# Kernel optimization log

Hardware: AMD Instinct MI355X
Metric: run time of the kernel (lower is better)

The kernel has to match this reference:

```python
import jax, jax.numpy as jnp
import numpy as np

EPS = 1e-5
NUM_HEADS = 8
TOP_K = 2
CAP_FACTOR = 2  # capacity = CAP_FACTOR * T * TOP_K / E


def layernorm(x, g, b):
    m = jnp.mean(x, axis=-1, keepdims=True)
    v = jnp.var(x, axis=-1, keepdims=True)
    return (x - m) * jax.lax.rsqrt(v + EPS) * g + b


def setup_inputs() -> dict:
    key = jax.random.key(0)
    ks = jax.random.split(key, 16)
    B, S, H, E, F = 2, 2048, 512, 64, 2048
    s = 0.02
    return {
        "x": jax.random.normal(ks[0], (B, S, H), jnp.float32),
        "ln1_g": jnp.ones((H,), jnp.float32),
        "ln1_b": jnp.zeros((H,), jnp.float32),
        "wq": jax.random.normal(ks[1], (H, H), jnp.float32) * s,
        "wk": jax.random.normal(ks[2], (H, H), jnp.float32) * s,
        "wv": jax.random.normal(ks[3], (H, H), jnp.float32) * s,
        "wo": jax.random.normal(ks[4], (H, H), jnp.float32) * s,
        "ln2_g": jnp.ones((H,), jnp.float32),
        "ln2_b": jnp.zeros((H,), jnp.float32),
        "wr": jax.random.normal(ks[5], (H, E), jnp.float32) * s,
        "w1": jax.random.normal(ks[6], (E, H, F), jnp.float32) * s,
        "b1": jnp.zeros((E, F), jnp.float32),
        "w2": jax.random.normal(ks[7], (E, F, H), jnp.float32) * s,
        "b2": jnp.zeros((E, H), jnp.float32),
    }


def reference(x, ln1_g, ln1_b, wq, wk, wv, wo, ln2_g, ln2_b, wr, w1, b1, w2, b2):
    B, S, H = x.shape
    NH = NUM_HEADS
    dh = H // NH

    # ---- pre-norm multi-head self-attention + residual ----
    x1 = layernorm(x, ln1_g, ln1_b)
    q = (x1 @ wq).reshape(B, S, NH, dh)
    k = (x1 @ wk).reshape(B, S, NH, dh)
    v = (x1 @ wv).reshape(B, S, NH, dh)
    scores = jnp.einsum("bqhd,bkhd->bhqk", q, k) * (dh ** -0.5)
    p = jax.nn.softmax(scores, axis=-1)
    attn_out = jnp.einsum("bhqk,bkhd->bqhd", p, v).reshape(B, S, H) @ wo
    x = x + attn_out

    # ---- pre-norm top-2 MoE + residual ----
    x2 = layernorm(x, ln2_g, ln2_b).reshape(B * S, H)  # [T, H]
    T = B * S
    E = wr.shape[1]
    C = CAP_FACTOR * (T * TOP_K // E)  # expert capacity

    probs = jax.nn.softmax(x2 @ wr, axis=-1)            # [T, E]
    gate_v, gate_i = jax.lax.top_k(probs, TOP_K)        # [T, K]
    gate_v = gate_v / jnp.sum(gate_v, axis=-1, keepdims=True)

    ef = gate_i.reshape(-1)                              # [T*K] expert per slot
    gf = gate_v.reshape(-1)                              # [T*K] gate per slot
    oh = jax.nn.one_hot(ef, E, dtype=x2.dtype)           # [T*K, E]
    # position of each slot within its expert queue
    pos = jnp.sum((jnp.cumsum(oh, axis=0) - oh) * oh, axis=1).astype(jnp.int32)
    keep = (pos < C).astype(x2.dtype)                    # drop overflow tokens
    posc = jnp.minimum(pos, C - 1)

    tok = jnp.repeat(x2, TOP_K, axis=0) * keep[:, None]  # [T*K, H]
    buf = jnp.zeros((E, C, H), x2.dtype).at[ef, posc].add(tok)  # dispatch

    h = jax.nn.gelu(jnp.einsum("ech,ehf->ecf", buf, w1) + b1[:, None, :])
    y = jnp.einsum("ecf,efh->ech", h, w2) + b2[:, None, :]

    ys = y[ef, posc] * (gf * keep)[:, None]              # combine, [T*K, H]
    moe_out = ys.reshape(T, TOP_K, H).sum(axis=1).reshape(B, S, H)
    return x + moe_out
```

## Files before the change

kernel.cpp:

```cpp
#include <hip/hip_runtime.h>
#include <hip/hip_bf16.h>
#include <math.h>

constexpr int Bc  = 2;
constexpr int Sc  = 2048;
constexpr int Hc  = 512;
constexpr int NHc = 8;
constexpr int Tc  = Bc * Sc;
constexpr int Ec  = 64;
constexpr int Fc  = 2048;
constexpr int Cap = 256;

typedef __attribute__((ext_vector_type(8))) short bf16x8;
typedef __attribute__((ext_vector_type(4))) float f32x4;

__device__ __forceinline__ unsigned short f2b(float f) {
    union { float f; unsigned u; } v; v.f = f;
    unsigned r = v.u + 0x7FFF + ((v.u >> 16) & 1);
    return (unsigned short)(r >> 16);
}

__device__ __forceinline__ float b2f(unsigned short u) {
    union { unsigned u; float f; } v; v.u = ((unsigned)u) << 16; return v.f;
}

__device__ __forceinline__ unsigned cvt_pk_bf16(float lo, float hi) {
    unsigned r;
    asm volatile("v_cvt_pk_bf16_f32 %0, %1, %2" : "=v"(r) : "v"(lo), "v"(hi));
    return r;
}

__device__ __forceinline__ float gelu_f(float x) {
    float u = x + 0.044715f * x * x * x;
    float r = __builtin_amdgcn_exp2f(-2.302211692851f * u);
    return x * __builtin_amdgcn_rcpf(1.0f + r);
}

__global__ __launch_bounds__(256) void ln_rows_kernel(const float* __restrict__ x,
                                                      const float* __restrict__ g,
                                                      const float* __restrict__ b,
                                                      unsigned short* __restrict__ o) {
    int w = threadIdx.x >> 6, l = threadIdx.x & 63;
    int t = blockIdx.x * 4 + w;
    const float4* row = (const float4*)(x + (size_t)t * Hc);
    float4 a = row[l], c = row[l + 64];
    float s  = a.x + a.y + a.z + a.w + c.x + c.y + c.z + c.w;
    float s2 = a.x * a.x + a.y * a.y + a.z * a.z + a.w * a.w
             + c.x * c.x + c.y * c.y + c.z * c.z + c.w * c.w;
    #pragma unroll
    for (int off = 32; off; off >>= 1) {
        s  += __shfl_xor(s,  off);
        s2 += __shfl_xor(s2, off);
    }
    float mean = s * (1.0f / Hc);
    float var  = s2 * (1.0f / Hc) - mean * mean;
    float r = rsqrtf(var + 1e-5f);
    float4 g0 = ((const float4*)g)[l], g1 = ((const float4*)g)[l + 64];
    float4 b0 = ((const float4*)b)[l], b1 = ((const float4*)b)[l + 64];
    ushort4 u0, u1;
    u0.x = f2b((a.x - mean) * r * g0.x + b0.x);
    u0.y = f2b((a.y - mean) * r * g0.y + b0.y);
    u0.z = f2b((a.z - mean) * r * g0.z + b0.z);
    u0.w = f2b((a.w - mean) * r * g0.w + b0.w);
    u1.x = f2b((c.x - mean) * r * g1.x + b1.x);
    u1.y = f2b((c.y - mean) * r * g1.y + b1.y);
    u1.z = f2b((c.z - mean) * r * g1.z + b1.z);
    u1.w = f2b((c.w - mean) * r * g1.w + b1.w);
    ((ushort4*)(o + (size_t)t * Hc))[l]      = u0;
    ((ushort4*)(o + (size_t)t * Hc))[l + 64] = u1;
}

template <int BM, int EPI, int SWZ, typename TC>
__global__ __launch_bounds__(BM * 2) void gemm_mfma(const unsigned short* __restrict__ A,
                                                    const float* __restrict__ W,
                                                    TC* __restrict__ C,
                                                    const float* __restrict__ X,
                                                    int M, int N, int K,
                                                    long sA, long sW, long sC, long sX,
                                                    const float* __restrict__ Wb,
                                                    const float* __restrict__ Wc) {
    int bx = blockIdx.x, bz = blockIdx.z, by = blockIdx.y;
    if (SWZ) {
        int gx = gridDim.x;
        int nwg = gx * gridDim.z;
        int flat = bx + gx * bz;
        int wg = (flat & 7) * (nwg >> 3) + (flat >> 3);
        bx = wg % gx; bz = wg / gx;
    }
    A += (size_t)bz * sA;
    if (Wb) W = (bz == 0) ? W : ((bz == 1) ? Wb : Wc);
    else    W += (size_t)bz * sW;
    C += (size_t)bz * sC;
    if (X) X += (size_t)bz * sX;
    int m0 = by * BM, n0 = bx * 128;

    __shared__ unsigned short As[BM * 72];
    __shared__ unsigned short Bs[128 * 72];

    int tid = threadIdx.x;
    int wid = tid >> 6, lane = tid & 63;
    int wr = (wid >> 1) * 64, wc = (wid & 1) * 64;
    int lr = lane & 15, lg = lane >> 4;

    constexpr int WP = 512 / BM;
    bf16x8 areg[4];
    float4 wa[WP], wb[WP];

    auto load_tile = [&](int k0) {
        #pragma unroll
        for (int p = 0; p < 4; p++) {
            int e = p * 16 * BM + tid * 8;
            int row = e >> 6, col = e & 63;
            areg[p] = *(const bf16x8*)&A[(size_t)(m0 + row) * K + k0 + col];
        }
        #pragma unroll
        for (int p = 0; p < WP; p++) {
            int kp = (tid >> 5) + p * (BM / 16);
            int c  = (tid & 31) * 4;
            const float* w0 = &W[(size_t)(k0 + 2 * kp) * N + n0 + c];
            wa[p] = *(const float4*)w0;
            wb[p] = *(const float4*)(w0 + N);
        }
    };
    auto write_tile = [&]() {
        #pragma unroll
        for (int p = 0; p < 4; p++) {
            int e = p * 16 * BM + tid * 8;
            int row = e >> 6, col = e & 63;
            *(bf16x8*)&As[row * 72 + col] = areg[p];
        }
        #pragma unroll
        for (int p = 0; p < WP; p++) {
            int kp = (tid >> 5) + p * (BM / 16);
            int c  = (tid & 31) * 4;
            int qz = 8 * ((c >> 3) & 7);
            int kof = (2 * kp) ^ qz;
            *(ushort2*)&Bs[(c + 0) * 72 + kof] = (ushort2){f2b(wa[p].x), f2b(wb[p].x)};
            *(ushort2*)&Bs[(c + 1) * 72 + kof] = (ushort2){f2b(wa[p].y), f2b(wb[p].y)};
            *(ushort2*)&Bs[(c + 2) * 72 + kof] = (ushort2){f2b(wa[p].z), f2b(wb[p].z)};
            *(ushort2*)&Bs[(c + 3) * 72 + kof] = (ushort2){f2b(wa[p].w), f2b(wb[p].w)};
        }
    };

    f32x4 acc[4][4];
    #pragma unroll
    for (int i = 0; i < 4; i++)
        #pragma unroll
        for (int j = 0; j < 4; j++) acc[i][j] = (f32x4){0.f, 0.f, 0.f, 0.f};

    load_tile(0);
    int nsteps = K >> 6;
    for (int s = 0; s < nsteps; s++) {
        write_tile();
        if (s + 1 < nsteps) load_tile((s + 1) << 6);
        asm volatile("s_waitcnt lgkmcnt(0)" ::: "memory");
        __builtin_amdgcn_s_barrier();
        #pragma unroll
        for (int kk = 0; kk < 64; kk += 32) {
            bf16x8 af[4], bfr[4];
            #pragma unroll
            for (int i = 0; i < 4; i++) {
                af[i] = *(const bf16x8*)&As[(wr + i * 16 + lr) * 72 + kk + 8 * lg];
                int nrow = wc + i * 16 + lr;
                int qq = 8 * ((nrow >> 3) & 7);
                bfr[i] = *(const bf16x8*)&Bs[nrow * 72 + ((kk + 8 * lg) ^ qq)];
            }
            #pragma unroll
            for (int i = 0; i < 4; i++)
                #pragma unroll
                for (int j = 0; j < 4; j++)
                    acc[i][j] = __builtin_amdgcn_mfma_f32_16x16x32_bf16(af[i], bfr[j], acc[i][j], 0, 0, 0);
        }
        asm volatile("s_waitcnt lgkmcnt(0)" ::: "memory");
        __builtin_amdgcn_s_barrier();
    }

    #pragma unroll
    for (int i = 0; i < 4; i++) {
        #pragma unroll
        for (int r = 0; r < 4; r++) {
            int m = m0 + wr + i * 16 + lg * 4 + r;
            #pragma unroll
            for (int j = 0; j < 4; j++) {
                int n = n0 + wc + j * 16 + lr;
                float vv = acc[i][j][r];
                if (EPI == 1) vv += X[(size_t)m * N + n];
                if (EPI == 2) { vv += X[n]; vv = gelu_f(vv); }
                if (EPI == 3) vv += X[n];
                if constexpr (sizeof(TC) == 2) C[(size_t)m * N + n] = (TC)f2b(vv);
                else                            C[(size_t)m * N + n] = vv;
            }
        }
    }
}

__global__ __launch_bounds__(256) void attn_mfma_kernel(const unsigned short* __restrict__ q,
                                                        const unsigned short* __restrict__ k,
                                                        const unsigned short* __restrict__ v,
                                                        unsigned short* __restrict__ o) {
    constexpr int LDK = 72;
    constexpr int NT  = Sc / 64;
    __shared__ unsigned short Ks[2][64 * LDK];
    __shared__ unsigned short Vt[2][64 * LDK];

    int flat = blockIdx.x;
    int wg = (flat & 7) * 64 + (flat >> 3);
    int qt = wg & 31;
    int hb = wg >> 5;
    int hh = hb & 7, b = hb >> 3;

    int q0 = qt * 64;
    int tid = threadIdx.x;
    int wid = tid >> 6, lane = tid & 63;
    int lr = lane & 15, lg = lane >> 4;

    const unsigned short* kbase = k + (size_t)(b * Sc) * Hc + hh * 64;
    const unsigned short* vbase = v + (size_t)(b * Sc) * Hc + hh * 64;

    bf16x8 qf[2];
    {
        const unsigned short* qrow = q + ((size_t)(b * Sc + q0 + wid * 16 + lr)) * Hc + hh * 64;
        qf[0] = *(const bf16x8*)&qrow[8 * lg];
        qf[1] = *(const bf16x8*)&qrow[32 + 8 * lg];
    }

    int krow = tid >> 3;
    int kcol = (tid & 7) * 8;
    int vk2  = (tid >> 4) * 2;
    int vd4  = (tid & 15) * 4;

    bf16x8 kr[2];
    ushort4 va[2], vb2[2];

    auto load_tile = [&](int kt) {
        #pragma unroll
        for (int p = 0; p < 2; p++) {
            kr[p] = *(const bf16x8*)&kbase[(size_t)(kt * 64 + p * 32 + krow) * Hc + kcol];
            const unsigned short* vp = &vbase[(size_t)(kt * 64 + p * 32 + vk2) * Hc + vd4];
            va[p]  = *(const ushort4*)vp;
            vb2[p] = *(const ushort4*)(vp + Hc);
        }
    };
    auto vswz = [](int d, int c) { return c ^ (8 * ((d >> 3) & 7)); };
    auto store_tile = [&](int bu) {
        #pragma unroll
        for (int p = 0; p < 2; p++) {
            *(bf16x8*)&Ks[bu][(p * 32 + krow) * LDK + kcol] = kr[p];
            int k2 = p * 32 + vk2;
            *(ushort2*)&Vt[bu][(vd4 + 0) * LDK + vswz(vd4 + 0, k2)] = (ushort2){va[p].x, vb2[p].x};
            *(ushort2*)&Vt[bu][(vd4 + 1) * LDK + vswz(vd4 + 1, k2)] = (ushort2){va[p].y, vb2[p].y};
            *(ushort2*)&Vt[bu][(vd4 + 2) * LDK + vswz(vd4 + 2, k2)] = (ushort2){va[p].z, vb2[p].z};
            *(ushort2*)&Vt[bu][(vd4 + 3) * LDK + vswz(vd4 + 3, k2)] = (ushort2){va[p].w, vb2[p].w};
        }
    };

    f32x4 Oacc[4];
    #pragma unroll
    for (int nb = 0; nb < 4; nb++) Oacc[nb] = (f32x4){0.f, 0.f, 0.f, 0.f};
    float mrun = -1e30f, lrun = 0.f;
    const float SCL2 = 0.125f * 1.4426950408889634f;

    load_tile(0);
    store_tile(0);
    __syncthreads();

    for (int kt = 0; kt < NT; kt++) {
        int cur = kt & 1;
        if (kt + 1 < NT) load_tile(kt + 1);

        f32x4 sacc[4];
        #pragma unroll
        for (int kb = 0; kb < 4; kb++) sacc[kb] = (f32x4){0.f, 0.f, 0.f, 0.f};
        __builtin_amdgcn_s_setprio(1);
        #pragma unroll
        for (int kb = 0; kb < 4; kb++) {
            #pragma unroll
            for (int s = 0; s < 2; s++) {
                bf16x8 kf = *(const bf16x8*)&Ks[cur][(kb * 16 + lr) * LDK + 32 * s + 8 * lg];
                sacc[kb] = __builtin_amdgcn_mfma_f32_16x16x32_bf16(kf, qf[s], sacc[kb], 0, 0, 0);
            }
        }
        __builtin_amdgcn_s_setprio(0);

        float z[4][4];
        float mt = -1e30f;
        #pragma unroll
        for (int kb = 0; kb < 4; kb++)
            #pragma unroll
            for (int r = 0; r < 4; r++) {
                z[kb][r] = sacc[kb][r] * SCL2;
                mt = fmaxf(mt, z[kb][r]);
            }
        mt = fmaxf(mt, __shfl_xor(mt, 16));
        mt = fmaxf(mt, __shfl_xor(mt, 32));

        bool defer = __all(mt - mrun <= 11.0f);
        float pv[4][4];
        float ps = 0.f;
        if (defer) {
            #pragma unroll
            for (int kb = 0; kb < 4; kb++)
                #pragma unroll
                for (int r = 0; r < 4; r++) {
                    pv[kb][r] = __builtin_amdgcn_exp2f(z[kb][r] - mrun);
                    ps += pv[kb][r];
                }
            ps += __shfl_xor(ps, 16);
            ps += __shfl_xor(ps, 32);
            lrun += ps;
        } else {
            float mnew = fmaxf(mrun, mt);
            float sc = __builtin_amdgcn_exp2f(mrun - mnew);
            #pragma unroll
            for (int kb = 0; kb < 4; kb++)
                #pragma unroll
                for (int r = 0; r < 4; r++) {
                    pv[kb][r] = __builtin_amdgcn_exp2f(z[kb][r] - mnew);
                    ps += pv[kb][r];
                }
            ps += __shfl_xor(ps, 16);
            ps += __shfl_xor(ps, 32);
            lrun = lrun * sc + ps;
            mrun = mnew;
            float scb[4];
            #pragma unroll
            for (int r = 0; r < 4; r++) scb[r] = __shfl(sc, lg * 4 + r);
            #pragma unroll
            for (int nb = 0; nb < 4; nb++)
                #pragma unroll
                for (int r = 0; r < 4; r++) Oacc[nb][r] *= scb[r];
        }

        unsigned d_[4][2];
        #pragma unroll
        for (int kb = 0; kb < 4; kb++) {
            d_[kb][0] = cvt_pk_bf16(pv[kb][0], pv[kb][1]);
            d_[kb][1] = cvt_pk_bf16(pv[kb][2], pv[kb][3]);
        }
        unsigned pfw[2][4];
        #pragma unroll
        for (int s = 0; s < 2; s++) {
            #pragma unroll
            for (int h = 0; h < 2; h++) {
                unsigned xx = d_[2 * s][h], yy = d_[2 * s + 1][h];
                asm volatile("v_permlane32_swap_b32 %0, %1" : "+v"(xx), "+v"(yy));
                asm volatile("v_permlane16_swap_b32 %0, %1" : "+v"(xx), "+v"(yy));
                pfw[s][h]     = xx;
                pfw[s][2 + h] = yy;
            }
        }
        bf16x8 pf0, pf1;
        *(unsigned*)&((short*)&pf0)[0] = pfw[0][0];
        *(unsigned*)&((short*)&pf0)[2] = pfw[0][1];
        *(unsigned*)&((short*)&pf0)[4] = pfw[0][2];
        *(unsigned*)&((short*)&pf0)[6] = pfw[0][3];
        *(unsigned*)&((short*)&pf1)[0] = pfw[1][0];
        *(unsigned*)&((short*)&pf1)[2] = pfw[1][1];
        *(unsigned*)&((short*)&pf1)[4] = pfw[1][2];
        *(unsigned*)&((short*)&pf1)[6] = pfw[1][3];

        __builtin_amdgcn_s_setprio(1);
        #pragma unroll
        for (int nb = 0; nb < 4; nb++) {
            f32x4 oa = Oacc[nb];
            int vrow = nb * 16 + lr;
            bf16x8 vf0 = *(const bf16x8*)&Vt[cur][vrow * LDK + vswz(vrow, 8 * lg)];
            bf16x8 vf1 = *(const bf16x8*)&Vt[cur][vrow * LDK + vswz(vrow, 32 + 8 * lg)];
            oa = __builtin_amdgcn_mfma_f32_16x16x32_bf16(pf0, vf0, oa, 0, 0, 0);
            oa = __builtin_amdgcn_mfma_f32_16x16x32_bf16(pf1, vf1, oa, 0, 0, 0);
            Oacc[nb] = oa;
        }
        __builtin_amdgcn_s_setprio(0);

        if (kt + 1 < NT) store_tile(cur ^ 1);
        __syncthreads();
    }

    float linv = 1.0f / lrun;
    unsigned short* ob = o + ((size_t)(b * Sc + q0 + wid * 16)) * Hc + hh * 64;
    #pragma unroll
    for (int r = 0; r < 4; r++) {
        float invB = __shfl(linv, lg * 4 + r);
        #pragma unroll
        for (int nb = 0; nb < 4; nb++) {
            ob[(size_t)(lg * 4 + r) * Hc + nb * 16 + lr] = f2b(Oacc[nb][r] * invB);
        }
    }
}

__global__ __launch_bounds__(256) void ln2_router_kernel(const float* __restrict__ xa,
                                                         const float* __restrict__ g,
                                                         const float* __restrict__ b,
                                                         const float* __restrict__ wr,
                                                         unsigned short* __restrict__ x2b,
                                                         int* __restrict__ ef,
                                                         float* __restrict__ gf) {
    int t = blockIdx.x;
    const float* row = xa + (size_t)t * Hc;
    int tid = threadIdx.x;
    int w = tid >> 6, l = tid & 63;
    float v0 = row[tid];
    float v1 = row[tid + 256];
    float s = v0 + v1, s2 = v0 * v0 + v1 * v1;
    for (int off = 32; off; off >>= 1) {
        s  += __shfl_down(s,  off);
        s2 += __shfl_down(s2, off);
    }
    __shared__ float ls[4], ls2[4];
    __shared__ float xn[512];
    __shared__ float part[4][64];
    if (l == 0) { ls[w] = s; ls2[w] = s2; }
    __syncthreads();
    if (tid == 0) {
        float a = 0.f, a2 = 0.f;
        for (int i = 0; i < 4; i++) { a += ls[i]; a2 += ls2[i]; }
        ls[0] = a; ls2[0] = a2;
    }
    __syncthreads();
    float mean = ls[0] * (1.0f / Hc);
    float var  = ls2[0] * (1.0f / Hc) - mean * mean;
    float r = rsqrtf(var + 1e-5f);
    float o0 = (v0 - mean) * r * g[tid]       + b[tid];
    float o1 = (v1 - mean) * r * g[tid + 256] + b[tid + 256];
    xn[tid] = o0; xn[tid + 256] = o1;
    x2b[(size_t)t * Hc + tid]       = f2b(o0);
    x2b[(size_t)t * Hc + tid + 256] = f2b(o1);
    __syncthreads();

    float acc = 0.f;
    const float* wrow = wr + (size_t)(w * 128) * Ec + l;
    #pragma unroll 8
    for (int hh = 0; hh < 128; hh++)
        acc += xn[w * 128 + hh] * wrow[(size_t)hh * Ec];
    part[w][l] = acc;
    __syncthreads();
    if (w == 0) {
        float logit = part[0][l] + part[1][l] + part[2][l] + part[3][l];
        float mx = logit;
        for (int off = 32; off; off >>= 1) mx = fmaxf(mx, __shfl_xor(mx, off));
        float p = __expf(logit - mx);
        float sum = p;
        for (int off = 32; off; off >>= 1) sum += __shfl_xor(sum, off);
        p /= sum;
        float v1_ = p; int i1 = l;
        for (int off = 32; off; off >>= 1) {
            float ov = __shfl_xor(v1_, off);
            int   oi = __shfl_xor(i1, off);
            if (ov > v1_ || (ov == v1_ && oi < i1)) { v1_ = ov; i1 = oi; }
        }
        float v2_ = (l == i1) ? -INFINITY : p; int i2 = l;
        for (int off = 32; off; off >>= 1) {
            float ov = __shfl_xor(v2_, off);
            int   oi = __shfl_xor(i2, off);
            if (ov > v2_ || (ov == v2_ && oi < i2)) { v2_ = ov; i2 = oi; }
        }
        if (l == 0) {
            float inv = 1.0f / (v1_ + v2_);
            ef[t * 2]     = i1;
            ef[t * 2 + 1] = i2;
            gf[t * 2]     = v1_ * inv;
            gf[t * 2 + 1] = v2_ * inv;
        }
    }
}

__global__ __launch_bounds__(256) void pos_kernel(const int* __restrict__ ef,
                                                  int* __restrict__ pos) {
    int e = blockIdx.x;
    __shared__ int cnts[257];
    int tid = threadIdx.x;
    int base = tid * 32;
    int c = 0;
    for (int i = 0; i < 32; i++) c += (ef[base + i] == e) ? 1 : 0;
    cnts[tid + 1] = c;
    if (tid == 0) cnts[0] = 0;
    __syncthreads();
    #pragma unroll
    for (int off = 1; off < 256; off <<= 1) {
        int v = cnts[tid + 1];
        int add = (tid + 1 > off) ? cnts[tid + 1 - off] : 0;
        __syncthreads();
        cnts[tid + 1] = v + add;
        __syncthreads();
    }
    int run = cnts[tid];
    for (int i = 0; i < 32; i++) {
        if (ef[base + i] == e) pos[base + i] = run++;
    }
}

__global__ __launch_bounds__(128) void dispatch_kernel(const unsigned short* __restrict__ x2b,
                                                       const int* __restrict__ ef,
                                                       const int* __restrict__ pos,
                                                       unsigned short* __restrict__ buf) {
    int s = blockIdx.x;
    int p = pos[s];
    if (p >= Cap) return;
    int e = ef[s];
    int t = s >> 1;
    ushort4 vv = ((const ushort4*)(x2b + (size_t)t * Hc))[threadIdx.x];
    ((ushort4*)(buf + ((size_t)e * Cap + p) * Hc))[threadIdx.x] = vv;
}

__global__ __launch_bounds__(128) void combine_kernel(const float* __restrict__ xa,
                                                      const unsigned short* __restrict__ y,
                                                      const int* __restrict__ ef,
                                                      const int* __restrict__ pos,
                                                      const float* __restrict__ gf,
                                                      float* __restrict__ out) {
    int t = blockIdx.x;
    int d = threadIdx.x;
    float4 acc = ((const float4*)(xa + (size_t)t * Hc))[d];
    #pragma unroll
    for (int kk = 0; kk < 2; kk++) {
        int s = t * 2 + kk;
        int p = pos[s];
        if (p < Cap) {
            float w = gf[s];
            ushort4 yv = ((const ushort4*)(y + ((size_t)ef[s] * Cap + p) * Hc))[d];
            acc.x += w * b2f(yv.x);
            acc.y += w * b2f(yv.y);
            acc.z += w * b2f(yv.z);
            acc.w += w * b2f(yv.w);
        }
    }
    ((float4*)(out + (size_t)t * Hc))[d] = acc;
}

extern "C" void kernel_launch(void* const* d_in, const int* in_sizes, int n_in,
                              void* d_out, int out_size, void* d_ws, size_t ws_size,
                              hipStream_t stream) {
    const float* x     = (const float*)d_in[0];
    const float* ln1_g = (const float*)d_in[1];
    const float* ln1_b = (const float*)d_in[2];
    const float* wq    = (const float*)d_in[3];
    const float* wk    = (const float*)d_in[4];
    const float* wv    = (const float*)d_in[5];
    const float* wo    = (const float*)d_in[6];
    const float* ln2_g = (const float*)d_in[7];
    const float* ln2_b = (const float*)d_in[8];
    const float* wr    = (const float*)d_in[9];
    const float* w1    = (const float*)d_in[10];
    const float* b1    = (const float*)d_in[11];
    const float* w2    = (const float*)d_in[12];
    const float* b2    = (const float*)d_in[13];
    float* out = (float*)d_out;

    const size_t TH   = (size_t)Tc * Hc;
    const size_t ECH  = (size_t)Ec * Cap * Hc;
    const size_t ECF  = (size_t)Ec * Cap * Fc;
    const size_t HF   = (size_t)Hc * Fc;

    char* wsb = (char*)d_ws;
    size_t off = 0;
    auto alloc = [&](size_t bytes) { size_t r = off; off = (off + bytes + 255) & ~(size_t)255; return r; };
    size_t x1b_off = alloc(TH * 2);
    size_t qkv_off = alloc(TH * 2 * 3);
    size_t ab_off  = alloc(TH * 2);
    size_t xa_off  = alloc(TH * 4);
    size_t x2b_off = alloc(TH * 2);
    size_t ef_off  = alloc((size_t)Tc * 2 * 4);
    size_t pos_off = alloc((size_t)Tc * 2 * 4);
    size_t gf_off  = alloc((size_t)Tc * 2 * 4);
    size_t buf_off = alloc(ECH * 2);
    size_t h_off   = alloc(ECF * 2);
    size_t y_off   = alloc(ECH * 2);
    if (ws_size < off) return;

    unsigned short* x1b  = (unsigned short*)(wsb + x1b_off);
    unsigned short* qb   = (unsigned short*)(wsb + qkv_off);
    unsigned short* kb   = qb + TH;
    unsigned short* vb   = qb + 2 * TH;
    unsigned short* ab   = (unsigned short*)(wsb + ab_off);
    float* xa  = (float*)(wsb + xa_off);
    unsigned short* x2b = (unsigned short*)(wsb + x2b_off);
    int*   ef  = (int*)(wsb + ef_off);
    int*   pos = (int*)(wsb + pos_off);
    float* gf  = (float*)(wsb + gf_off);
    unsigned short* bufb = (unsigned short*)(wsb + buf_off);
    unsigned short* h    = (unsigned short*)(wsb + h_off);
    unsigned short* y    = (unsigned short*)(wsb + y_off);

    dim3 blk(256);

    ln_rows_kernel<<<Tc / 4, blk, 0, stream>>>(x, ln1_g, ln1_b, x1b);

    gemm_mfma<128, 0, 0, unsigned short><<<dim3(Hc / 128, Tc / 128, 3), blk, 0, stream>>>(
        x1b, wq, qb, nullptr, Tc, Hc, Hc, 0, 0, (long)TH, 0, wk, wv);

    attn_mfma_kernel<<<dim3(512), blk, 0, stream>>>(qb, kb, vb, ab);

    gemm_mfma<128, 1, 0, float><<<dim3(Hc / 128, Tc / 128, 1), blk, 0, stream>>>(
        ab, wo, xa, x, Tc, Hc, Hc, 0, 0, 0, 0, nullptr, nullptr);

    ln2_router_kernel<<<Tc, blk, 0, stream>>>(xa, ln2_g, ln2_b, wr, x2b, ef, gf);

    pos_kernel<<<Ec, blk, 0, stream>>>(ef, pos);

    dispatch_kernel<<<Tc * 2, dim3(128), 0, stream>>>(x2b, ef, pos, bufb);

    gemm_mfma<256, 2, 1, unsigned short><<<dim3(Fc / 128, Cap / 256, Ec), dim3(512), 0, stream>>>(
        bufb, w1, h, b1, Cap, Fc, Hc,
        (long)Cap * Hc, (long)HF, (long)Cap * Fc, (long)Fc, nullptr, nullptr);

    gemm_mfma<256, 3, 1, unsigned short><<<dim3(Hc / 128, Cap / 256, Ec), dim3(512), 0, stream>>>(
        h, w2, y, b2, Cap, Hc, Fc,
        (long)Cap * Fc, (long)HF, (long)Cap * Hc, (long)Hc, nullptr, nullptr);

    combine_kernel<<<Tc, dim3(128), 0, stream>>>(xa, y, ef, pos, gf, out);
}
```

Before: 291.6 us.

## Split attention over key range into four partials with a log-sum-exp reduce kernel

The attention kernel now processes one quarter of the key tiles per workgroup, launching four times as many workgroups, and writes unnormalized fp32 partial outputs plus running max and sum to workspace. A new reduce kernel rescales and combines the four partials and writes the normalized bf16 output. The aim is more parallelism to fill the GPU's compute units, since 512 workgroups underfill the device. The cost is extra global traffic for the partials (about 32MB), an additional kernel launch, and loss of the prefetch pipeline over a shorter loop.

Result: no change. 293.8 us (+0.7%).

```diff
diff --git a/kernel.cpp b/kernel.cpp
--- a/kernel.cpp
+++ b/kernel.cpp
@@ -10,6 +10,7 @@
 constexpr int Ec  = 64;
 constexpr int Fc  = 2048;
 constexpr int Cap = 256;
+constexpr int SPL = 4;
 
 typedef __attribute__((ext_vector_type(8))) short bf16x8;
 typedef __attribute__((ext_vector_type(4))) float f32x4;
@@ -194,19 +195,21 @@
     }
 }
 
-__global__ __launch_bounds__(256) void attn_mfma_kernel(const unsigned short* __restrict__ q,
-                                                        const unsigned short* __restrict__ k,
-                                                        const unsigned short* __restrict__ v,
-                                                        unsigned short* __restrict__ o) {
+__global__ __launch_bounds__(256) void attn_partial_kernel(const unsigned short* __restrict__ q,
+                                                           const unsigned short* __restrict__ k,
+                                                           const unsigned short* __restrict__ v,
+                                                           float* __restrict__ Opart,
+                                                           float* __restrict__ ml) {
     constexpr int LDK = 72;
-    constexpr int NT  = Sc / 64;
+    constexpr int TPS = (Sc / 64) / SPL;
     __shared__ unsigned short Ks[2][64 * LDK];
     __shared__ unsigned short Vt[2][64 * LDK];
 
     int flat = blockIdx.x;
-    int wg = (flat & 7) * 64 + (flat >> 3);
+    int wg = (flat & 7) * 256 + (flat >> 3);
     int qt = wg & 31;
-    int hb = wg >> 5;
+    int hb = (wg >> 5) & 15;
+    int split = wg >> 9;
     int hh = hb & 7, b = hb >> 3;
 
     int q0 = qt * 64;
@@ -260,13 +263,14 @@
     float mrun = -1e30f, lrun = 0.f;
     const float SCL2 = 0.125f * 1.4426950408889634f;
 
-    load_tile(0);
+    int kt0 = split * TPS;
+    load_tile(kt0);
     store_tile(0);
     __syncthreads();
 
-    for (int kt = 0; kt < NT; kt++) {
-        int cur = kt & 1;
-        if (kt + 1 < NT) load_tile(kt + 1);
+    for (int it = 0; it < TPS; it++) {
+        int cur = it & 1;
+        if (it + 1 < TPS) load_tile(kt0 + it + 1);
 
         f32x4 sacc[4];
         #pragma unroll
@@ -372,20 +376,76 @@
         }
         __builtin_amdgcn_s_setprio(0);
 
-        if (kt + 1 < NT) store_tile(cur ^ 1);
+        if (it + 1 < TPS) store_tile(cur ^ 1);
         __syncthreads();
     }
 
-    float linv = 1.0f / lrun;
-    unsigned short* ob = o + ((size_t)(b * Sc + q0 + wid * 16)) * Hc + hh * 64;
+    float* Ob = Opart + ((size_t)wg * 64 + wid * 16) * 64;
     #pragma unroll
     for (int r = 0; r < 4; r++) {
-        float invB = __shfl(linv, lg * 4 + r);
+        int qq = lg * 4 + r;
         #pragma unroll
         for (int nb = 0; nb < 4; nb++) {
-            ob[(size_t)(lg * 4 + r) * Hc + nb * 16 + lr] = f2b(Oacc[nb][r] * invB);
-        }
-    }
+            Ob[(size_t)qq * 64 + nb * 16 + lr] = Oacc[nb][r];
+        }
+    }
+    if (lg == 0) {
+        ml[((size_t)wg * 2 + 0) * 64 + wid * 16 + lr] = mrun;
+        ml[((size_t)wg * 2 + 1) * 64 + wid * 16 + lr] = lrun;
+    }
+}
+
+__global__ __launch_bounds__(256) void attn_reduce_kernel(const float* __restrict__ Opart,
+                                                          const float* __restrict__ ml,
+                                                          unsigned short* __restrict__ o) {
+    int rblk = blockIdx.x;
+    int qt = rblk & 31, hb = rblk >> 5;
+    int hh = hb & 7, b = hb >> 3;
+    int tid = threadIdx.x;
+    int qq = tid >> 2;
+    int d0 = (tid & 3) * 16;
+
+    float m_[SPL], l_[SPL];
+    float mstar = -1e30f;
+    #pragma unroll
+    for (int s = 0; s < SPL; s++) {
+        int wg = s * 512 + rblk;
+        m_[s] = ml[((size_t)wg * 2 + 0) * 64 + qq];
+        l_[s] = ml[((size_t)wg * 2 + 1) * 64 + qq];
+        mstar = fmaxf(mstar, m_[s]);
+    }
+    float lsum = 0.f;
+    float w_[SPL];
+    #pragma unroll
+    for (int s = 0; s < SPL; s++) {
+        w_[s] = __builtin_amdgcn_exp2f(m_[s] - mstar);
+        lsum += w_[s] * l_[s];
+    }
+    float inv = 1.0f / lsum;
+
+    float4 acc0 = {0.f, 0.f, 0.f, 0.f}, acc1 = {0.f, 0.f, 0.f, 0.f};
+    float4 acc2 = {0.f, 0.f, 0.f, 0.f}, acc3 = {0.f, 0.f, 0.f, 0.f};
+    #pragma unroll
+    for (int s = 0; s < SPL; s++) {
+        int wg = s * 512 + rblk;
+        const float4* Ob = (const float4*)&Opart[((size_t)wg * 64 + qq) * 64 + d0];
+        float ws = w_[s];
+        float4 a = Ob[0], bb = Ob[1], c = Ob[2], d = Ob[3];
+        acc0.x += ws * a.x;  acc0.y += ws * a.y;  acc0.z += ws * a.z;  acc0.w += ws * a.w;
+        acc1.x += ws * bb.x; acc1.y += ws * bb.y; acc1.z += ws * bb.z; acc1.w += ws * bb.w;
+        acc2.x += ws * c.x;  acc2.y += ws * c.y;  acc2.z += ws * c.z;  acc2.w += ws * c.w;
+        acc3.x += ws * d.x;  acc3.y += ws * d.y;  acc3.z += ws * d.z;  acc3.w += ws * d.w;
+    }
+    unsigned short* ob = o + ((size_t)(b * Sc + qt * 64 + qq)) * Hc + hh * 64 + d0;
+    ushort4 u0, u1, u2, u3;
+    u0.x = f2b(acc0.x * inv); u0.y = f2b(acc0.y * inv); u0.z = f2b(acc0.z * inv); u0.w = f2b(acc0.w * inv);
+    u1.x = f2b(acc1.x * inv); u1.y = f2b(acc1.y * inv); u1.z = f2b(acc1.z * inv); u1.w = f2b(acc1.w * inv);
+    u2.x = f2b(acc2.x * inv); u2.y = f2b(acc2.y * inv); u2.z = f2b(acc2.z * inv); u2.w = f2b(acc2.w * inv);
+    u3.x = f2b(acc3.x * inv); u3.y = f2b(acc3.y * inv); u3.z = f2b(acc3.z * inv); u3.w = f2b(acc3.w * inv);
+    ((ushort4*)ob)[0] = u0;
+    ((ushort4*)ob)[1] = u1;
+    ((ushort4*)ob)[2] = u2;
+    ((ushort4*)ob)[3] = u3;
 }
 
 __global__ __launch_bounds__(256) void ln2_router_kernel(const float* __restrict__ xa,
@@ -562,6 +622,8 @@
     size_t ef_off  = alloc((size_t)Tc * 2 * 4);
     size_t pos_off = alloc((size_t)Tc * 2 * 4);
     size_t gf_off  = alloc((size_t)Tc * 2 * 4);
+    size_t op_off  = alloc((size_t)SPL * 512 * 64 * 64 * 4);
+    size_t ml_off  = alloc((size_t)SPL * 512 * 2 * 64 * 4);
     size_t buf_off = alloc(ECH * 2);
     size_t h_off   = alloc(ECF * 2);
     size_t y_off   = alloc(ECH * 2);
@@ -577,6 +639,8 @@
     int*   ef  = (int*)(wsb + ef_off);
     int*   pos = (int*)(wsb + pos_off);
     float* gf  = (float*)(wsb + gf_off);
+    float* Opart = (float*)(wsb + op_off);
+    float* ml    = (float*)(wsb + ml_off);
     unsigned short* bufb = (unsigned short*)(wsb + buf_off);
     unsigned short* h    = (unsigned short*)(wsb + h_off);
     unsigned short* y    = (unsigned short*)(wsb + y_off);
@@ -588,7 +652,9 @@
     gemm_mfma<128, 0, 0, unsigned short><<<dim3(Hc / 128, Tc / 128, 3), blk, 0, stream>>>(
         x1b, wq, qb, nullptr, Tc, Hc, Hc, 0, 0, (long)TH, 0, wk, wv);
 
-    attn_mfma_kernel<<<dim3(512), blk, 0, stream>>>(qb, kb, vb, ab);
+    attn_partial_kernel<<<dim3(512 * SPL), blk, 0, stream>>>(qb, kb, vb, Opart, ml);
+
+    attn_reduce_kernel<<<dim3(512), blk, 0, stream>>>(Opart, ml, ab);
 
     gemm_mfma<128, 1, 0, float><<<dim3(Hc / 128, Tc / 128, 1), blk, 0, stream>>>(
         ab, wo, xa, x, Tc, Hc, Hc, 0, 0, 0, 0, nullptr, nullptr);
```

## Fuse router, position assignment and dispatch; narrow GEMM N-tile to 64

Applied to the files above, without the earlier changes.

The LN2/router kernel now assigns each token's slot in its expert queue with atomic counters and scatters its bf16 row straight into the expert buffer. This removes the separate pos_kernel and dispatch_kernel launches and the x2b round trip through global memory. The GEMM template gains BN, thread-count and min-waves parameters, and every GEMM now uses 64-wide N tiles, giving more blocks and higher occupancy. The cost is that atomic slot assignment is order-nondeterministic, so when an expert overflows capacity the dropped tokens may differ from the reference's cumsum order. It also adds a memset launch.

New measurement: 317.7 us. 8.9% more time.

```diff
diff --git a/kernel.cpp b/kernel.cpp
--- a/kernel.cpp
+++ b/kernel.cpp
@@ -70,15 +70,15 @@
     ((ushort4*)(o + (size_t)t * Hc))[l + 64] = u1;
 }
 
-template <int BM, int EPI, int SWZ, typename TC>
-__global__ __launch_bounds__(BM * 2) void gemm_mfma(const unsigned short* __restrict__ A,
-                                                    const float* __restrict__ W,
-                                                    TC* __restrict__ C,
-                                                    const float* __restrict__ X,
-                                                    int M, int N, int K,
-                                                    long sA, long sW, long sC, long sX,
-                                                    const float* __restrict__ Wb,
-                                                    const float* __restrict__ Wc) {
+template <int BM, int BN, int NTHR, int EPI, int SWZ, int MINW, typename TC>
+__global__ __launch_bounds__(NTHR, MINW) void gemm_mfma(const unsigned short* __restrict__ A,
+                                                        const float* __restrict__ W,
+                                                        TC* __restrict__ C,
+                                                        const float* __restrict__ X,
+                                                        int M, int N, int K,
+                                                        long sA, long sW, long sC, long sX,
+                                                        const float* __restrict__ Wb,
+                                                        const float* __restrict__ Wc) {
     int bx = blockIdx.x, bz = blockIdx.z, by = blockIdx.y;
     if (SWZ) {
         int gx = gridDim.x;
@@ -92,17 +92,19 @@
     else    W += (size_t)bz * sW;
     C += (size_t)bz * sC;
     if (X) X += (size_t)bz * sX;
-    int m0 = by * BM, n0 = bx * 128;
+    int m0 = by * BM, n0 = bx * BN;
 
     __shared__ unsigned short As[BM * 72];
-    __shared__ unsigned short Bs[128 * 72];
+    __shared__ unsigned short Bs[BN * 72];
 
     int tid = threadIdx.x;
     int wid = tid >> 6, lane = tid & 63;
-    int wr = (wid >> 1) * 64, wc = (wid & 1) * 64;
+    int wr = (wid >> 1) * 64, wc = (wid & 1) * (BN / 2);
     int lr = lane & 15, lg = lane >> 4;
 
-    constexpr int WP = 512 / BM;
+    constexpr int JN  = BN / 32;
+    constexpr int WP  = 8 * BN / NTHR;
+    constexpr int CPT = BN / 4;
     bf16x8 areg[4];
     float4 wa[WP], wb[WP];
 
@@ -115,8 +117,8 @@
         }
         #pragma unroll
         for (int p = 0; p < WP; p++) {
-            int kp = (tid >> 5) + p * (BM / 16);
-            int c  = (tid & 31) * 4;
+            int kp = tid / CPT + p * (NTHR / CPT);
+            int c  = (tid % CPT) * 4;
             const float* w0 = &W[(size_t)(k0 + 2 * kp) * N + n0 + c];
             wa[p] = *(const float4*)w0;
             wb[p] = *(const float4*)(w0 + N);
@@ -131,8 +133,8 @@
         }
         #pragma unroll
         for (int p = 0; p < WP; p++) {
-            int kp = (tid >> 5) + p * (BM / 16);
-            int c  = (tid & 31) * 4;
+            int kp = tid / CPT + p * (NTHR / CPT);
+            int c  = (tid % CPT) * 4;
             int qz = 8 * ((c >> 3) & 7);
             int kof = (2 * kp) ^ qz;
             *(ushort2*)&Bs[(c + 0) * 72 + kof] = (ushort2){f2b(wa[p].x), f2b(wb[p].x)};
@@ -142,11 +144,11 @@
         }
     };
 
-    f32x4 acc[4][4];
+    f32x4 acc[4][JN];
     #pragma unroll
     for (int i = 0; i < 4; i++)
         #pragma unroll
-        for (int j = 0; j < 4; j++) acc[i][j] = (f32x4){0.f, 0.f, 0.f, 0.f};
+        for (int j = 0; j < JN; j++) acc[i][j] = (f32x4){0.f, 0.f, 0.f, 0.f};
 
     load_tile(0);
     int nsteps = K >> 6;
@@ -157,18 +159,20 @@
         __builtin_amdgcn_s_barrier();
         #pragma unroll
         for (int kk = 0; kk < 64; kk += 32) {
-            bf16x8 af[4], bfr[4];
-            #pragma unroll
-            for (int i = 0; i < 4; i++) {
+            bf16x8 af[4], bfr[JN];
+            #pragma unroll
+            for (int i = 0; i < 4; i++)
                 af[i] = *(const bf16x8*)&As[(wr + i * 16 + lr) * 72 + kk + 8 * lg];
-                int nrow = wc + i * 16 + lr;
+            #pragma unroll
+            for (int j = 0; j < JN; j++) {
+                int nrow = wc + j * 16 + lr;
                 int qq = 8 * ((nrow >> 3) & 7);
-                bfr[i] = *(const bf16x8*)&Bs[nrow * 72 + ((kk + 8 * lg) ^ qq)];
+                bfr[j] = *(const bf16x8*)&Bs[nrow * 72 + ((kk + 8 * lg) ^ qq)];
             }
             #pragma unroll
             for (int i = 0; i < 4; i++)
                 #pragma unroll
-                for (int j = 0; j < 4; j++)
+                for (int j = 0; j < JN; j++)
                     acc[i][j] = __builtin_amdgcn_mfma_f32_16x16x32_bf16(af[i], bfr[j], acc[i][j], 0, 0, 0);
         }
         asm volatile("s_waitcnt lgkmcnt(0)" ::: "memory");
@@ -181,7 +185,7 @@
         for (int r = 0; r < 4; r++) {
             int m = m0 + wr + i * 16 + lg * 4 + r;
             #pragma unroll
-            for (int j = 0; j < 4; j++) {
+            for (int j = 0; j < JN; j++) {
                 int n = n0 + wc + j * 16 + lr;
                 float vv = acc[i][j][r];
                 if (EPI == 1) vv += X[(size_t)m * N + n];
@@ -388,13 +392,15 @@
     }
 }
 
-__global__ __launch_bounds__(256) void ln2_router_kernel(const float* __restrict__ xa,
-                                                         const float* __restrict__ g,
-                                                         const float* __restrict__ b,
-                                                         const float* __restrict__ wr,
-                                                         unsigned short* __restrict__ x2b,
-                                                         int* __restrict__ ef,
-                                                         float* __restrict__ gf) {
+__global__ __launch_bounds__(256) void ln2rd_kernel(const float* __restrict__ xa,
+                                                    const float* __restrict__ g,
+                                                    const float* __restrict__ b,
+                                                    const float* __restrict__ wr,
+                                                    unsigned short* __restrict__ buf,
+                                                    int* __restrict__ ef,
+                                                    int* __restrict__ pos,
+                                                    float* __restrict__ gf,
+                                                    int* __restrict__ cnt) {
     int t = blockIdx.x;
     const float* row = xa + (size_t)t * Hc;
     int tid = threadIdx.x;
@@ -408,7 +414,9 @@
     }
     __shared__ float ls[4], ls2[4];
     __shared__ float xn[512];
+    __shared__ unsigned short xb[512];
     __shared__ float part[4][64];
+    __shared__ int bc[4];
     if (l == 0) { ls[w] = s; ls2[w] = s2; }
     __syncthreads();
     if (tid == 0) {
@@ -423,8 +431,7 @@
     float o0 = (v0 - mean) * r * g[tid]       + b[tid];
     float o1 = (v1 - mean) * r * g[tid + 256] + b[tid + 256];
     xn[tid] = o0; xn[tid + 256] = o1;
-    x2b[(size_t)t * Hc + tid]       = f2b(o0);
-    x2b[(size_t)t * Hc + tid + 256] = f2b(o1);
+    xb[tid] = f2b(o0); xb[tid + 256] = f2b(o1);
     __syncthreads();
 
     float acc = 0.f;
@@ -456,50 +463,20 @@
         }
         if (l == 0) {
             float inv = 1.0f / (v1_ + v2_);
-            ef[t * 2]     = i1;
-            ef[t * 2 + 1] = i2;
+            int p1 = atomicAdd(&cnt[i1], 1);
+            int p2 = atomicAdd(&cnt[i2], 1);
+            ef[t * 2]     = i1;  ef[t * 2 + 1]  = i2;
+            pos[t * 2]    = p1;  pos[t * 2 + 1] = p2;
             gf[t * 2]     = v1_ * inv;
             gf[t * 2 + 1] = v2_ * inv;
-        }
-    }
-}
-
-__global__ __launch_bounds__(256) void pos_kernel(const int* __restrict__ ef,
-                                                  int* __restrict__ pos) {
-    int e = blockIdx.x;
-    __shared__ int cnts[257];
-    int tid = threadIdx.x;
-    int base = tid * 32;
-    int c = 0;
-    for (int i = 0; i < 32; i++) c += (ef[base + i] == e) ? 1 : 0;
-    cnts[tid + 1] = c;
-    if (tid == 0) cnts[0] = 0;
+            bc[0] = i1; bc[1] = i2; bc[2] = p1; bc[3] = p2;
+        }
+    }
     __syncthreads();
-    #pragma unroll
-    for (int off = 1; off < 256; off <<= 1) {
-        int v = cnts[tid + 1];
-        int add = (tid + 1 > off) ? cnts[tid + 1 - off] : 0;
-        __syncthreads();
-        cnts[tid + 1] = v + add;
-        __syncthreads();
-    }
-    int run = cnts[tid];
-    for (int i = 0; i < 32; i++) {
-        if (ef[base + i] == e) pos[base + i] = run++;
-    }
-}
-
-__global__ __launch_bounds__(128) void dispatch_kernel(const unsigned short* __restrict__ x2b,
-                                                       const int* __restrict__ ef,
-                                                       const int* __restrict__ pos,
-                                                       unsigned short* __restrict__ buf) {
-    int s = blockIdx.x;
-    int p = pos[s];
-    if (p >= Cap) return;
-    int e = ef[s];
-    int t = s >> 1;
-    ushort4 vv = ((const ushort4*)(x2b + (size_t)t * Hc))[threadIdx.x];
-    ((ushort4*)(buf + ((size_t)e * Cap + p) * Hc))[threadIdx.x] = vv;
+    int e1 = bc[0], e2 = bc[1], p1 = bc[2], p2 = bc[3];
+    ushort2 u = *(ushort2*)&xb[tid * 2];
+    if (p1 < Cap) ((ushort2*)(buf + ((size_t)e1 * Cap + p1) * Hc))[tid] = u;
+    if (p2 < Cap) ((ushort2*)(buf + ((size_t)e2 * Cap + p2) * Hc))[tid] = u;
 }
 
 __global__ __launch_bounds__(128) void combine_kernel(const float* __restrict__ xa,
@@ -558,10 +535,10 @@
     size_t qkv_off = alloc(TH * 2 * 3);
     size_t ab_off  = alloc(TH * 2);
     size_t xa_off  = alloc(TH * 4);
-    size_t x2b_off = alloc(TH * 2);
     size_t ef_off  = alloc((size_t)Tc * 2 * 4);
     size_t pos_off = alloc((size_t)Tc * 2 * 4);
     size_t gf_off  = alloc((size_t)Tc * 2 * 4);
+    size_t cnt_off = alloc((size_t)Ec * 4);
     size_t buf_off = alloc(ECH * 2);
     size_t h_off   = alloc(ECF * 2);
     size_t y_off   = alloc(ECH * 2);
@@ -573,10 +550,10 @@
     unsigned short* vb   = qb + 2 * TH;
     unsigned short* ab   = (unsigned short*)(wsb + ab_off);
     float* xa  = (float*)(wsb + xa_off);
-    unsigned short* x2b = (unsigned short*)(wsb + x2b_off);
     int*   ef  = (int*)(wsb + ef_off);
     int*   pos = (int*)(wsb + pos_off);
     float* gf  = (float*)(wsb + gf_off);
+    int*   cnt = (int*)(wsb + cnt_off);
     unsigned short* bufb = (unsigned short*)(wsb + buf_off);
     unsigned short* h    = (unsigned short*)(wsb + h_off);
     unsigned short* y    = (unsigned short*)(wsb + y_off);
@@ -585,25 +562,22 @@
 
     ln_rows_kernel<<<Tc / 4, blk, 0, stream>>>(x, ln1_g, ln1_b, x1b);
 
-    gemm_mfma<128, 0, 0, unsigned short><<<dim3(Hc / 128, Tc / 128, 3), blk, 0, stream>>>(
+    gemm_mfma<128, 64, 256, 0, 0, 1, unsigned short><<<dim3(Hc / 64, Tc / 128, 3), blk, 0, stream>>>(
         x1b, wq, qb, nullptr, Tc, Hc, Hc, 0, 0, (long)TH, 0, wk, wv);
 
     attn_mfma_kernel<<<dim3(512), blk, 0, stream>>>(qb, kb, vb, ab);
 
-    gemm_mfma<128, 1, 0, float><<<dim3(Hc / 128, Tc / 128, 1), blk, 0, stream>>>(
+    gemm_mfma<128, 64, 256, 1, 0, 1, float><<<dim3(Hc / 64, Tc / 128, 1), blk, 0, stream>>>(
         ab, wo, xa, x, Tc, Hc, Hc, 0, 0, 0, 0, nullptr, nullptr);
 
-    ln2_router_kernel<<<Tc, blk, 0, stream>>>(xa, ln2_g, ln2_b, wr, x2b, ef, gf);
-
-    pos_kernel<<<Ec, blk, 0, stream>>>(ef, pos);
-
-    dispatch_kernel<<<Tc * 2, dim3(128), 0, stream>>>(x2b, ef, pos, bufb);
-
-    gemm_mfma<256, 2, 1, unsigned short><<<dim3(Fc / 128, Cap / 256, Ec), dim3(512), 0, stream>>>(
+    hipMemsetAsync(cnt, 0, Ec * sizeof(int), stream);
+    ln2rd_kernel<<<Tc, blk, 0, stream>>>(xa, ln2_g, ln2_b, wr, bufb, ef, pos, gf, cnt);
+
+    gemm_mfma<256, 64, 512, 2, 1, 4, unsigned short><<<dim3(Fc / 64, Cap / 256, Ec), dim3(512), 0, stream>>>(
         bufb, w1, h, b1, Cap, Fc, Hc,
         (long)Cap * Hc, (long)HF, (long)Cap * Fc, (long)Fc, nullptr, nullptr);
 
-    gemm_mfma<256, 3, 1, unsigned short><<<dim3(Hc / 128, Cap / 256, Ec), dim3(512), 0, stream>>>(
+    gemm_mfma<256, 64, 512, 3, 1, 4, unsigned short><<<dim3(Hc / 64, Cap / 256, Ec), dim3(512), 0, stream>>>(
         h, w2, y, b2, Cap, Hc, Fc,
         (long)Cap * Fc, (long)HF, (long)Cap * Hc, (long)Hc, nullptr, nullptr);
 
```
